# Kernel tuning notes

Measured on AMD Instinct MI355X. Metric: run time of the kernel, lower is better.

## Reference

```python
import jax, jax.numpy as jnp
import numpy as np

IN_F = 8192
OUT_F = 8192
MAX_STATES = 100
THRESHOLD = MAX_STATES // 2  # 50


def setup_inputs() -> dict:
    key = jax.random.key(0)
    k1, k2 = jax.random.split(key, 2)
    spike_input = (jax.random.uniform(k1, (IN_F,)) < 0.2).astype(jnp.float32)
    # synapse states as in __init__: randn*5 + threshold, clamped to [1, max_states]
    synapse_states = jnp.clip(
        jax.random.normal(k2, (OUT_F, IN_F)) * 5.0 + THRESHOLD, 1.0, float(MAX_STATES)
    ).astype(jnp.float32)
    membrane_potential = jnp.zeros((OUT_F,), jnp.float32)
    adaptive_threshold = jnp.full((OUT_F,), 3.0, jnp.float32)
    eligibility_trace = jnp.zeros((OUT_F, IN_F), jnp.float32)
    refractory_period = jnp.zeros((OUT_F,), jnp.float32)
    return {
        "spike_input": spike_input,
        "synapse_states": synapse_states,
        "membrane_potential": membrane_potential,
        "adaptive_threshold": adaptive_threshold,
        "eligibility_trace": eligibility_trace,
        "refractory_period": refractory_period,
    }


def reference(spike_input, synapse_states, membrane_potential, adaptive_threshold,
              eligibility_trace, refractory_period):
    # Ternary (effectively binary 0/1) weights from synapse states
    w = (synapse_states > float(THRESHOLD)).astype(jnp.float32)  # [out, in]
    x = spike_input.reshape(-1)                                   # [in]
    current = w @ x                                               # [out]
    # LIF membrane update with refractory gating
    v_mem = membrane_potential * 0.5 + current * (1.0 - refractory_period * 0.5)
    spikes = (v_mem >= adaptive_threshold).astype(jnp.float32)    # [out]
    # Eligibility trace: decay + outer-product accumulation + clamp
    new_trace = jnp.clip(eligibility_trace * 0.8 + jnp.outer(spikes, x), 0.0, 5.0)
    # Refractory update
    new_refractory = jnp.clip(refractory_period + spikes - 0.1, 0.0, 1.0)
    # Membrane reset where spiked
    new_membrane = v_mem * (1.0 - spikes)
    return spikes, new_membrane, new_trace, new_refractory
```

## Files before the change

### kernel.cpp

```cpp
#include <hip/hip_runtime.h>


#define IN_F 8192
#define OUT_F 8192
#define BLOCK 256

__global__ __launch_bounds__(BLOCK) void snn_matvec_kernel(
    const float4* __restrict__ x4,
    const float* __restrict__ syn,
    const float* __restrict__ mem,
    const float* __restrict__ thr,
    const float* __restrict__ refr,
    float* __restrict__ out_spikes,
    float* __restrict__ out_mem,
    float* __restrict__ out_refr)
{
    const int wave = threadIdx.x >> 6;
    const int lane = threadIdx.x & 63;
    const int row  = (blockIdx.x << 2) + wave;

    const float4* __restrict__ syn4 =
        (const float4*)(syn + (size_t)row * IN_F);

    float acc = 0.0f;
    #pragma unroll 8
    for (int it = 0; it < IN_F / 4 / 64; ++it) {
        const int idx = (it << 6) + lane;
        const float4 s  = syn4[idx];
        const float4 xv = x4[idx];
        acc += (s.x > 50.0f) ? xv.x : 0.0f;
        acc += (s.y > 50.0f) ? xv.y : 0.0f;
        acc += (s.z > 50.0f) ? xv.z : 0.0f;
        acc += (s.w > 50.0f) ? xv.w : 0.0f;
    }
    #pragma unroll
    for (int off = 32; off > 0; off >>= 1) {
        acc += __shfl_down(acc, off, 64);
    }
    if (lane == 0) {
        const float r = refr[row];
        const float v = mem[row] * 0.5f + acc * (1.0f - r * 0.5f);
        const float spike = (v >= thr[row]) ? 1.0f : 0.0f;
        out_spikes[row] = spike;
        out_mem[row]    = v * (1.0f - spike);
        out_refr[row]   = fminf(fmaxf(r + spike - 0.1f, 0.0f), 1.0f);
    }
}

__global__ __launch_bounds__(BLOCK) void snn_trace_kernel(
    const float4* __restrict__ x4,
    const float4* __restrict__ tr4,
    const float* __restrict__ spikes,
    float4* __restrict__ otr4)
{
    const int row = blockIdx.x;
    const float spike = spikes[row];
    const size_t base = (size_t)row * (IN_F / 4);

    #pragma unroll
    for (int it = 0; it < IN_F / 4 / BLOCK; ++it) {
        const int idx = it * BLOCK + threadIdx.x;
        const float4 t  = tr4[base + idx];
        const float4 xv = x4[idx];
        float4 o;
        o.x = fminf(fmaxf(t.x * 0.8f + spike * xv.x, 0.0f), 5.0f);
        o.y = fminf(fmaxf(t.y * 0.8f + spike * xv.y, 0.0f), 5.0f);
        o.z = fminf(fmaxf(t.z * 0.8f + spike * xv.z, 0.0f), 5.0f);
        o.w = fminf(fmaxf(t.w * 0.8f + spike * xv.w, 0.0f), 5.0f);
        otr4[base + idx] = o;
    }
}

extern "C" void kernel_launch(void* const* d_in, const int* in_sizes, int n_in,
                              void* d_out, int out_size, void* d_ws, size_t ws_size,
                              hipStream_t stream) {
    const float* x_in  = (const float*)d_in[0];
    const float* syn   = (const float*)d_in[1];
    const float* mem   = (const float*)d_in[2];
    const float* thr   = (const float*)d_in[3];
    const float* trace = (const float*)d_in[4];
    const float* refr  = (const float*)d_in[5];

    float* out = (float*)d_out;
    float* out_spikes = out;
    float* out_mem    = out + OUT_F;
    float* out_trace  = out + 2 * OUT_F;
    float* out_refr   = out + 2 * OUT_F + (size_t)OUT_F * IN_F;

    snn_matvec_kernel<<<OUT_F / 4, BLOCK, 0, stream>>>(
        (const float4*)x_in, syn, mem, thr, refr,
        out_spikes, out_mem, out_refr);

    snn_trace_kernel<<<OUT_F, BLOCK, 0, stream>>>(
        (const float4*)x_in, (const float4*)trace, out_spikes,
        (float4*)out_trace);
}
```

Measured before the change: 587.2 us.

## Fuse matvec and trace update into one wave-per-row kernel with nontemporal stores

The matvec and eligibility-trace kernels are merged so that each wave computes its row's spike and then updates that row's trace directly. This removes the second launch and the global round-trip of spikes between kernels, and lets trace traffic overlap with other waves' matvec reads. Trace output is written with nontemporal stores to avoid polluting cache. The cost is that each wave now serializes its matvec and trace phases, with less parallelism per row in the trace phase than the old block-per-row kernel.

After: 599.5 us. 2.1% more time.

```diff
diff --git a/kernel.cpp b/kernel.cpp
--- a/kernel.cpp
+++ b/kernel.cpp
@@ -4,30 +4,38 @@
 #define IN_F 8192
 #define OUT_F 8192
 #define BLOCK 256
+#define WAVE_ITERS (IN_F / 4 / 64)
 
-__global__ __launch_bounds__(BLOCK) void snn_matvec_kernel(
-    const float4* __restrict__ x4,
+typedef float vfloat4 __attribute__((ext_vector_type(4)));
+
+__global__ __launch_bounds__(BLOCK) void snn_wave_fused_kernel(
+    const vfloat4* __restrict__ x4,
     const float* __restrict__ syn,
     const float* __restrict__ mem,
     const float* __restrict__ thr,
+    const float* __restrict__ trace,
     const float* __restrict__ refr,
     float* __restrict__ out_spikes,
     float* __restrict__ out_mem,
+    float* __restrict__ out_trace,
     float* __restrict__ out_refr)
 {
     const int wave = threadIdx.x >> 6;
     const int lane = threadIdx.x & 63;
     const int row  = (blockIdx.x << 2) + wave;
 
-    const float4* __restrict__ syn4 =
-        (const float4*)(syn + (size_t)row * IN_F);
+    const vfloat4* __restrict__ syn4 =
+        (const vfloat4*)(syn + (size_t)row * IN_F);
+    const vfloat4* __restrict__ tr4 =
+        (const vfloat4*)(trace + (size_t)row * IN_F);
+    vfloat4* __restrict__ otr4 = (vfloat4*)(out_trace + (size_t)row * IN_F);
 
     float acc = 0.0f;
     #pragma unroll 8
-    for (int it = 0; it < IN_F / 4 / 64; ++it) {
+    for (int it = 0; it < WAVE_ITERS; ++it) {
         const int idx = (it << 6) + lane;
-        const float4 s  = syn4[idx];
-        const float4 xv = x4[idx];
+        const vfloat4 s  = syn4[idx];
+        const vfloat4 xv = x4[idx];
         acc += (s.x > 50.0f) ? xv.x : 0.0f;
         acc += (s.y > 50.0f) ? xv.y : 0.0f;
         acc += (s.z > 50.0f) ? xv.z : 0.0f;
@@ -37,37 +45,28 @@
     for (int off = 32; off > 0; off >>= 1) {
         acc += __shfl_down(acc, off, 64);
     }
+    const float current = __shfl(acc, 0, 64);
+
+    const float r = refr[row];
+    const float v = mem[row] * 0.5f + current * (1.0f - r * 0.5f);
+    const float spike = (v >= thr[row]) ? 1.0f : 0.0f;
     if (lane == 0) {
-        const float r = refr[row];
-        const float v = mem[row] * 0.5f + acc * (1.0f - r * 0.5f);
-        const float spike = (v >= thr[row]) ? 1.0f : 0.0f;
         out_spikes[row] = spike;
         out_mem[row]    = v * (1.0f - spike);
         out_refr[row]   = fminf(fmaxf(r + spike - 0.1f, 0.0f), 1.0f);
     }
-}
 
-__global__ __launch_bounds__(BLOCK) void snn_trace_kernel(
-    const float4* __restrict__ x4,
-    const float4* __restrict__ tr4,
-    const float* __restrict__ spikes,
-    float4* __restrict__ otr4)
-{
-    const int row = blockIdx.x;
-    const float spike = spikes[row];
-    const size_t base = (size_t)row * (IN_F / 4);
-
-    #pragma unroll
-    for (int it = 0; it < IN_F / 4 / BLOCK; ++it) {
-        const int idx = it * BLOCK + threadIdx.x;
-        const float4 t  = tr4[base + idx];
-        const float4 xv = x4[idx];
-        float4 o;
+    #pragma unroll 8
+    for (int it = 0; it < WAVE_ITERS; ++it) {
+        const int idx = (it << 6) + lane;
+        const vfloat4 t  = tr4[idx];
+        const vfloat4 xv = x4[idx];
+        vfloat4 o;
         o.x = fminf(fmaxf(t.x * 0.8f + spike * xv.x, 0.0f), 5.0f);
         o.y = fminf(fmaxf(t.y * 0.8f + spike * xv.y, 0.0f), 5.0f);
         o.z = fminf(fmaxf(t.z * 0.8f + spike * xv.z, 0.0f), 5.0f);
         o.w = fminf(fmaxf(t.w * 0.8f + spike * xv.w, 0.0f), 5.0f);
-        otr4[base + idx] = o;
+        __builtin_nontemporal_store(o, &otr4[idx]);
     }
 }
 
@@ -87,11 +86,7 @@
     float* out_trace  = out + 2 * OUT_F;
     float* out_refr   = out + 2 * OUT_F + (size_t)OUT_F * IN_F;
 
-    snn_matvec_kernel<<<OUT_F / 4, BLOCK, 0, stream>>>(
-        (const float4*)x_in, syn, mem, thr, refr,
-        out_spikes, out_mem, out_refr);
-
-    snn_trace_kernel<<<OUT_F, BLOCK, 0, stream>>>(
-        (const float4*)x_in, (const float4*)trace, out_spikes,
-        (float4*)out_trace);
+    snn_wave_fused_kernel<<<OUT_F / 4, BLOCK, 0, stream>>>(
+        (const vfloat4*)x_in, syn, mem, thr, trace, refr,
+        out_spikes, out_mem, out_trace, out_refr);
 }
```
